# Kernel tuning notes

Measured on AMD Instinct MI355X. Metric: run time of the kernel, lower is better.

## Reference

```python
import jax, jax.numpy as jnp
import numpy as np

B, N, IN_F, OUT_F, H = 16, 1024, 256, 256, 4
D = OUT_F // H  # head_dim = 64
NEG_SLOPE = 0.2


def setup_inputs() -> dict:
    key = jax.random.key(0)
    k1, k2, k3 = jax.random.split(key, 3)
    h = jax.random.normal(k1, (B, N, IN_F), dtype=jnp.float32)
    mask = jnp.ones((B, N), dtype=jnp.int32)
    W = jax.random.normal(k2, (OUT_F, IN_F), dtype=jnp.float32) * (1.0 / np.sqrt(IN_F))
    a = jax.random.normal(k3, (2 * D, 1), dtype=jnp.float32) * 0.1
    return {"h": h, "mask": mask, "W": W, "a": a}


def reference(h, mask, W, a):
    # Wh = h @ W.T -> (B, N, OUT_F) -> (B, H, N, D)
    Wh = jnp.einsum('bnf,of->bno', h, W)
    Wh = Wh.reshape(h.shape[0], h.shape[1], H, D).transpose(0, 2, 1, 3)
    # Additive split: cat([Wh_i, Wh_j]) @ a == Wh_i @ a1 + Wh_j @ a2 (same math,
    # avoids the O(N^2 * 2D) concat tensor)
    a1 = a[:D, 0]  # (D,)
    a2 = a[D:, 0]  # (D,)
    s1 = jnp.einsum('bhnd,d->bhn', Wh, a1)  # score for node i
    s2 = jnp.einsum('bhnd,d->bhn', Wh, a2)  # score for node j
    e = s1[:, :, :, None] + s2[:, :, None, :]          # (B, H, N, N)
    e = jnp.where(e >= 0, e, NEG_SLOPE * e)            # LeakyReLU(0.2)
    node_mask = mask.astype(bool)                      # (B, N)
    mm = node_mask[:, None, :, None] & node_mask[:, None, None, :]  # (B,1,N,N)
    e = jnp.where(mm, e, -jnp.inf)
    attn = jax.nn.softmax(e, axis=-1)
    # dropout is identity in eval mode
    attn = jnp.where(mm, attn, 0.0)
    h_prime = jnp.einsum('bhij,bhjd->bhid', attn, Wh)  # (B, H, N, D)
    h_prime = h_prime.transpose(0, 2, 1, 3).reshape(h.shape[0], h.shape[1], OUT_F)
    return h_prime * mask.astype(h_prime.dtype)[:, :, None]
```

## Files before the change

### kernel.cpp

```cpp
#include <hip/hip_runtime.h>

typedef short short8 __attribute__((ext_vector_type(8)));
typedef float floatx4 __attribute__((ext_vector_type(4)));
typedef float floatx16 __attribute__((ext_vector_type(16)));
typedef unsigned int u32;

#define NEG_SLOPE 0.2f

__device__ __forceinline__ u32 pk_rtne(float a, float b) {
    u32 ua = __float_as_uint(a); ua += 0x7fffu + ((ua >> 16) & 1u);
    u32 ub = __float_as_uint(b); ub += 0x7fffu + ((ub >> 16) & 1u);
    return __builtin_amdgcn_perm(ub, ua, 0x07060302);
}
__device__ __forceinline__ u32 pk_trunc(float a, float b) {
    return __builtin_amdgcn_perm(__float_as_uint(b), __float_as_uint(a), 0x07060302);
}
__device__ __forceinline__ void gl_lds16(const void* g, void* l) {
    __builtin_amdgcn_global_load_lds((__attribute__((address_space(1))) u32*)(void*)g,
                                     (__attribute__((address_space(3))) u32*)l, 16, 0, 0);
}

__global__ __launch_bounds__(256, 4) void k_wh(
    const float* __restrict__ hin, const int* __restrict__ mask,
    const float* __restrict__ W, const float* __restrict__ a,
    unsigned short* __restrict__ WhF, float2* __restrict__ E1F1,
    float2* __restrict__ E2F2)
{
    __shared__ unsigned short sBF[8 * 4 * 64 * 8];
    __shared__ float sV1[256], sV2[256];

    const int t = threadIdx.x;
    const int bi = blockIdx.x;
    const int mtile = bi & 255, hh = bi >> 8;
    const int m0g = mtile * 64;
    const int b = m0g >> 10, i0 = m0g & 1023;
    const int b4h = b * 4 + hh;
    const int wid = t >> 6, lane = t & 63;
    const int l15 = lane & 15, q = lane >> 4;

    sV1[t] = 0.f;
    sV2[t] = 0.f;
    __syncthreads();

    float vp1[8] = {0, 0, 0, 0, 0, 0, 0, 0};
    float vp2[8] = {0, 0, 0, 0, 0, 0, 0, 0};
    {
        const int c = t & 31;
        const int rb = t >> 5;
#pragma unroll
        for (int i = 0; i < 8; ++i) {
            int row = i * 8 + rb;
            const float* gp = &W[((size_t)(hh * 64 + row)) * 256 + c * 8];
            float4 w0 = *(const float4*)gp;
            float4 w1 = *(const float4*)(gp + 4);
            float a1r = a[row], a2r = a[64 + row];
            vp1[0] += a1r * w0.x; vp1[1] += a1r * w0.y; vp1[2] += a1r * w0.z; vp1[3] += a1r * w0.w;
            vp1[4] += a1r * w1.x; vp1[5] += a1r * w1.y; vp1[6] += a1r * w1.z; vp1[7] += a1r * w1.w;
            vp2[0] += a2r * w0.x; vp2[1] += a2r * w0.y; vp2[2] += a2r * w0.z; vp2[3] += a2r * w0.w;
            vp2[4] += a2r * w1.x; vp2[5] += a2r * w1.y; vp2[6] += a2r * w1.z; vp2[7] += a2r * w1.w;
            uint4 pv;
            pv.x = pk_rtne(w0.x, w0.y); pv.y = pk_rtne(w0.z, w0.w);
            pv.z = pk_rtne(w1.x, w1.y); pv.w = pk_rtne(w1.z, w1.w);
            int kt = c >> 2, qq = c & 3, nt = row >> 4, r15 = row & 15;
            int idx16 = (kt * 4 + nt) * 64 + qq * 16 + r15;
            *(uint4*)&sBF[(idx16 ^ kt) * 8] = pv;
        }
    }
#pragma unroll
    for (int j = 0; j < 8; ++j) {
        vp1[j] += __shfl_xor(vp1[j], 32, 64);
        vp2[j] += __shfl_xor(vp2[j], 32, 64);
    }
    if (lane < 32) {
        const int c = t & 31;
#pragma unroll
        for (int j = 0; j < 8; ++j) {
            atomicAdd(&sV1[c * 8 + j], vp1[j]);
            atomicAdd(&sV2[c * 8 + j], vp2[j]);
        }
    }
    __syncthreads();

    floatx4 acc[4];
#pragma unroll
    for (int nt = 0; nt < 4; ++nt) {
        floatx4 z = {0.f, 0.f, 0.f, 0.f};
        acc[nt] = z;
    }
    float s1a = 0.f, s2a = 0.f;
    const float* hrow = &hin[((size_t)(m0g + wid * 16 + l15)) * 256 + q * 8];
#pragma unroll
    for (int kt = 0; kt < 8; ++kt) {
        float4 h0 = *(const float4*)(hrow + kt * 32);
        float4 h1 = *(const float4*)(hrow + kt * 32 + 4);
        float4 v1a = *(const float4*)&sV1[kt * 32 + q * 8];
        float4 v1b = *(const float4*)&sV1[kt * 32 + q * 8 + 4];
        float4 v2a = *(const float4*)&sV2[kt * 32 + q * 8];
        float4 v2b = *(const float4*)&sV2[kt * 32 + q * 8 + 4];
        s1a += h0.x * v1a.x + h0.y * v1a.y + h0.z * v1a.z + h0.w * v1a.w
             + h1.x * v1b.x + h1.y * v1b.y + h1.z * v1b.z + h1.w * v1b.w;
        s2a += h0.x * v2a.x + h0.y * v2a.y + h0.z * v2a.z + h0.w * v2a.w
             + h1.x * v2b.x + h1.y * v2b.y + h1.z * v2b.z + h1.w * v2b.w;
        union { short8 s; uint4 u; } af;
        af.u.x = pk_rtne(h0.x, h0.y); af.u.y = pk_rtne(h0.z, h0.w);
        af.u.z = pk_rtne(h1.x, h1.y); af.u.w = pk_rtne(h1.z, h1.w);
#pragma unroll
        for (int nt = 0; nt < 4; ++nt) {
            int idx16 = (kt * 4 + nt) * 64 + lane;
            short8 bf = *(const short8*)&sBF[(idx16 ^ kt) * 8];
            acc[nt] = __builtin_amdgcn_mfma_f32_16x16x32_bf16(af.s, bf, acc[nt], 0, 0, 0);
        }
    }

    const int jt16 = (i0 >> 4) + wid;
    const int g = q & 1, jb = (q >> 1) * 4;
#pragma unroll
    for (int nt = 0; nt < 4; ++nt) {
        int nt32 = nt >> 1;
        int l31 = (nt & 1) * 16 + l15;
        uint2 pv;
        pv.x = pk_rtne(acc[nt][0], acc[nt][1]);
        pv.y = pk_rtne(acc[nt][2], acc[nt][3]);
        size_t idx = ((((size_t)b4h * 64 + jt16) * 2 + nt32) * 64 + (g * 32 + l31)) * 8 + jb;
        *(uint2*)&WhF[idx] = pv;
    }

    s1a += __shfl_xor(s1a, 16, 64); s1a += __shfl_xor(s1a, 32, 64);
    s2a += __shfl_xor(s2a, 16, 64); s2a += __shfl_xor(s2a, 32, 64);
    if (lane < 16) {
        int i = i0 + wid * 16 + lane;
        E1F1[(size_t)b4h * 1024 + i] = make_float2(__expf(s1a), __expf(NEG_SLOPE * s1a));
        int mj = mask[b * 1024 + i];
        E2F2[(size_t)b4h * 1024 + i] =
            make_float2(mj ? __expf(s2a) : 0.f, mj ? __expf(NEG_SLOPE * s2a) : 0.f);
    }
}

__global__ __launch_bounds__(256, 4) void k_attn(
    const int* __restrict__ mask,
    const unsigned short* __restrict__ WhF,
    const float2* __restrict__ E1F1, const float2* __restrict__ E2F2,
    float* __restrict__ out)
{
    __shared__ float2 sEF[1024];
    __shared__ float sRed[2][64][49];

    const int t = threadIdx.x;
    const int bi = blockIdx.x;
    const int b4h = bi & 63, ib = bi >> 6;
    const int b = b4h >> 2, hh = b4h & 3;
    const int i0 = ib * 64;
    const int wid = t >> 6, lane = t & 63;
    const int l31 = lane & 31, g = lane >> 5;
    const int rg = wid & 1, jh = wid >> 1;
    const int iw = i0 + rg * 32;

    {
        const char* src = (const char*)(E2F2 + (size_t)b4h * 1024);
        gl_lds16(src + t * 16, (char*)sEF + t * 16);
        gl_lds16(src + 4096 + t * 16, (char*)sEF + 4096 + t * 16);
    }

    float2 e1 = E1F1[(size_t)b4h * 1024 + iw + l31];
    const float E1 = e1.x, F1 = e1.y;

    floatx16 acc0, acc1, accL;
#pragma unroll
    for (int r = 0; r < 16; ++r) { acc0[r] = 0.f; acc1[r] = 0.f; accL[r] = 0.f; }
    const short ob = (short)0x3F80;
    const short8 ones = {ob, ob, ob, ob, ob, ob, ob, ob};

    const char* gbase = (const char*)WhF + (size_t)b4h * 131072 + (size_t)lane * 16;
    const int cb = jh * 32;

    short8 ga0 = *(const short8*)(gbase + (size_t)cb * 2048);
    short8 ga1 = *(const short8*)(gbase + (size_t)cb * 2048 + 1024);
    short8 gb0 = *(const short8*)(gbase + (size_t)(cb + 1) * 2048);
    short8 gb1 = *(const short8*)(gbase + (size_t)(cb + 1) * 2048 + 1024);

    __syncthreads();

    float4 nA0, nA1, nB0, nB1;
    {
        const float4* pA = (const float4*)&sEF[cb * 16 + g * 4];
        const float4* pB = (const float4*)&sEF[cb * 16 + 8 + g * 4];
        nA0 = pA[0]; nA1 = pA[1]; nB0 = pB[0]; nB1 = pB[1];
    }

#pragma unroll 4
    for (int cr = 0; cr < 32; cr += 2) {
        {
            const float4 eA0 = nA0, eA1 = nA1, eB0 = nB0, eB1 = nB1;
            const int cn = cb + ((cr + 1) & 31);
            const float4* pA = (const float4*)&sEF[cn * 16 + g * 4];
            const float4* pB = (const float4*)&sEF[cn * 16 + 8 + g * 4];
            nA0 = pA[0]; nA1 = pA[1]; nB0 = pB[0]; nB1 = pB[1];
            const short8 bf0 = ga0, bf1 = ga1;
            const int cg = cb + ((cr + 2) & 31);
            ga0 = *(const short8*)(gbase + (size_t)cg * 2048);
            ga1 = *(const short8*)(gbase + (size_t)cg * 2048 + 1024);
            float w0 = fmaxf(E1 * eA0.x, F1 * eA0.y);
            float w1 = fmaxf(E1 * eA0.z, F1 * eA0.w);
            float w2 = fmaxf(E1 * eA1.x, F1 * eA1.y);
            float w3 = fmaxf(E1 * eA1.z, F1 * eA1.w);
            float w4 = fmaxf(E1 * eB0.x, F1 * eB0.y);
            float w5 = fmaxf(E1 * eB0.z, F1 * eB0.w);
            float w6 = fmaxf(E1 * eB1.x, F1 * eB1.y);
            float w7 = fmaxf(E1 * eB1.z, F1 * eB1.w);
            union { short8 s; u32 u[4]; } af;
            af.u[0] = pk_trunc(w0, w1);
            af.u[1] = pk_trunc(w2, w3);
            af.u[2] = pk_trunc(w4, w5);
            af.u[3] = pk_trunc(w6, w7);
            acc0 = __builtin_amdgcn_mfma_f32_32x32x16_bf16(af.s, bf0, acc0, 0, 0, 0);
            acc1 = __builtin_amdgcn_mfma_f32_32x32x16_bf16(af.s, bf1, acc1, 0, 0, 0);
            accL = __builtin_amdgcn_mfma_f32_32x32x16_bf16(af.s, ones, accL, 0, 0, 0);
        }
        {
            const float4 eA0 = nA0, eA1 = nA1, eB0 = nB0, eB1 = nB1;
            const int cn = cb + ((cr + 2) & 31);
            const float4* pA = (const float4*)&sEF[cn * 16 + g * 4];
            const float4* pB = (const float4*)&sEF[cn * 16 + 8 + g * 4];
            nA0 = pA[0]; nA1 = pA[1]; nB0 = pB[0]; nB1 = pB[1];
            const short8 bf0 = gb0, bf1 = gb1;
            const int cg = cb + ((cr + 3) & 31);
            gb0 = *(const short8*)(gbase + (size_t)cg * 2048);
            gb1 = *(const short8*)(gbase + (size_t)cg * 2048 + 1024);
            float w0 = fmaxf(E1 * eA0.x, F1 * eA0.y);
            float w1 = fmaxf(E1 * eA0.z, F1 * eA0.w);
            float w2 = fmaxf(E1 * eA1.x, F1 * eA1.y);
            float w3 = fmaxf(E1 * eA1.z, F1 * eA1.w);
            float w4 = fmaxf(E1 * eB0.x, F1 * eB0.y);
            float w5 = fmaxf(E1 * eB0.z, F1 * eB0.w);
            float w6 = fmaxf(E1 * eB1.x, F1 * eB1.y);
            float w7 = fmaxf(E1 * eB1.z, F1 * eB1.w);
            union { short8 s; u32 u[4]; } af;
            af.u[0] = pk_trunc(w0, w1);
            af.u[1] = pk_trunc(w2, w3);
            af.u[2] = pk_trunc(w4, w5);
            af.u[3] = pk_trunc(w6, w7);
            acc0 = __builtin_amdgcn_mfma_f32_32x32x16_bf16(af.s, bf0, acc0, 0, 0, 0);
            acc1 = __builtin_amdgcn_mfma_f32_32x32x16_bf16(af.s, bf1, acc1, 0, 0, 0);
            accL = __builtin_amdgcn_mfma_f32_32x32x16_bf16(af.s, ones, accL, 0, 0, 0);
        }
    }

    if (jh == 1) {
        float* d = &sRed[rg][lane][0];
#pragma unroll
        for (int r = 0; r < 16; ++r) {
            d[r] = acc0[r]; d[16 + r] = acc1[r]; d[32 + r] = accL[r];
        }
    }
    __syncthreads();
    if (jh == 0) {
        const float* d = &sRed[rg][lane][0];
#pragma unroll
        for (int r = 0; r < 16; ++r) {
            acc0[r] += d[r]; acc1[r] += d[16 + r]; accL[r] += d[32 + r];
        }
#pragma unroll
        for (int r = 0; r < 16; ++r) {
            int row = (r & 3) + 8 * (r >> 2) + 4 * g;
            int i = iw + row;
            float l = accL[r];
            int mi = mask[b * 1024 + i];
            float inv = (mi && l > 0.f) ? 1.0f / l : 0.f;
            size_t o = ((size_t)(b * 1024 + i)) * 256 + hh * 64;
            out[o + l31] = acc0[r] * inv;
            out[o + 32 + l31] = acc1[r] * inv;
        }
    }
}

extern "C" void kernel_launch(void* const* d_in, const int* in_sizes, int n_in,
                              void* d_out, int out_size, void* d_ws, size_t ws_size,
                              hipStream_t stream) {
    const float* h = (const float*)d_in[0];
    const int* mask = (const int*)d_in[1];
    const float* W = (const float*)d_in[2];
    const float* a = (const float*)d_in[3];
    float* out = (float*)d_out;

    unsigned short* WhF = (unsigned short*)d_ws;
    float2* E1F1 = (float2*)((char*)d_ws + (size_t)64 * 64 * 2 * 64 * 8 * 2);
    float2* E2F2 = E1F1 + 64 * 1024;

    hipLaunchKernelGGL(k_wh, dim3(1024), dim3(256), 0, stream, h, mask, W, a, WhF, E1F1, E2F2);
    hipLaunchKernelGGL(k_attn, dim3(1024), dim3(256), 0, stream, mask, WhF, E1F1, E2F2, out);
}
```

Baseline: 103.2 us.

## Precompute bf16 W fragments and attention projection vectors in a separate prep kernel

Moves the per-head conversion of W to bf16 MFMA fragment layout and the W^T·a projection vectors into a small 4-block prep kernel that writes them to workspace. k_wh then reads B fragments and projection vectors straight from global memory instead of rebuilding them in LDS in every one of its 1024 blocks. This removes the redundant per-block W loads, reductions, atomics and barriers, but adds a kernel launch with little parallelism and makes the MFMA B operands come from global or cache rather than LDS.

```diff
diff --git a/kernel.cpp b/kernel.cpp
--- a/kernel.cpp
+++ b/kernel.cpp
@@ -20,15 +20,66 @@
                                      (__attribute__((address_space(3))) u32*)l, 16, 0, 0);
 }
 
+__global__ __launch_bounds__(256, 4) void k_prep(
+    const float* __restrict__ W, const float* __restrict__ a,
+    unsigned short* __restrict__ WFg, float* __restrict__ V1g,
+    float* __restrict__ V2g)
+{
+    __shared__ float sV1[256], sV2[256];
+    const int t = threadIdx.x;
+    const int hh = blockIdx.x;
+    const int lane = t & 63;
+
+    sV1[t] = 0.f;
+    sV2[t] = 0.f;
+    __syncthreads();
+
+    float vp1[8] = {0, 0, 0, 0, 0, 0, 0, 0};
+    float vp2[8] = {0, 0, 0, 0, 0, 0, 0, 0};
+    const int c = t & 31;
+    const int rb = t >> 5;
+#pragma unroll
+    for (int i = 0; i < 8; ++i) {
+        int row = i * 8 + rb;
+        const float* gp = &W[((size_t)(hh * 64 + row)) * 256 + c * 8];
+        float4 w0 = *(const float4*)gp;
+        float4 w1 = *(const float4*)(gp + 4);
+        float a1r = a[row], a2r = a[64 + row];
+        vp1[0] += a1r * w0.x; vp1[1] += a1r * w0.y; vp1[2] += a1r * w0.z; vp1[3] += a1r * w0.w;
+        vp1[4] += a1r * w1.x; vp1[5] += a1r * w1.y; vp1[6] += a1r * w1.z; vp1[7] += a1r * w1.w;
+        vp2[0] += a2r * w0.x; vp2[1] += a2r * w0.y; vp2[2] += a2r * w0.z; vp2[3] += a2r * w0.w;
+        vp2[4] += a2r * w1.x; vp2[5] += a2r * w1.y; vp2[6] += a2r * w1.z; vp2[7] += a2r * w1.w;
+        uint4 pv;
+        pv.x = pk_rtne(w0.x, w0.y); pv.y = pk_rtne(w0.z, w0.w);
+        pv.z = pk_rtne(w1.x, w1.y); pv.w = pk_rtne(w1.z, w1.w);
+        int kt = c >> 2, qq = c & 3, nt = row >> 4, r15 = row & 15;
+        int idx16 = (kt * 4 + nt) * 64 + qq * 16 + r15;
+        *(uint4*)&WFg[((size_t)hh * 2048 + idx16) * 8] = pv;
+    }
+#pragma unroll
+    for (int j = 0; j < 8; ++j) {
+        vp1[j] += __shfl_xor(vp1[j], 32, 64);
+        vp2[j] += __shfl_xor(vp2[j], 32, 64);
+    }
+    if (lane < 32) {
+#pragma unroll
+        for (int j = 0; j < 8; ++j) {
+            atomicAdd(&sV1[c * 8 + j], vp1[j]);
+            atomicAdd(&sV2[c * 8 + j], vp2[j]);
+        }
+    }
+    __syncthreads();
+    V1g[hh * 256 + t] = sV1[t];
+    V2g[hh * 256 + t] = sV2[t];
+}
+
 __global__ __launch_bounds__(256, 4) void k_wh(
     const float* __restrict__ hin, const int* __restrict__ mask,
-    const float* __restrict__ W, const float* __restrict__ a,
+    const unsigned short* __restrict__ WFg, const float* __restrict__ V1g,
+    const float* __restrict__ V2g,
     unsigned short* __restrict__ WhF, float2* __restrict__ E1F1,
     float2* __restrict__ E2F2)
 {
-    __shared__ unsigned short sBF[8 * 4 * 64 * 8];
-    __shared__ float sV1[256], sV2[256];
-
     const int t = threadIdx.x;
     const int bi = blockIdx.x;
     const int mtile = bi & 255, hh = bi >> 8;
@@ -38,49 +89,6 @@
     const int wid = t >> 6, lane = t & 63;
     const int l15 = lane & 15, q = lane >> 4;
 
-    sV1[t] = 0.f;
-    sV2[t] = 0.f;
-    __syncthreads();
-
-    float vp1[8] = {0, 0, 0, 0, 0, 0, 0, 0};
-    float vp2[8] = {0, 0, 0, 0, 0, 0, 0, 0};
-    {
-        const int c = t & 31;
-        const int rb = t >> 5;
-#pragma unroll
-        for (int i = 0; i < 8; ++i) {
-            int row = i * 8 + rb;
-            const float* gp = &W[((size_t)(hh * 64 + row)) * 256 + c * 8];
-            float4 w0 = *(const float4*)gp;
-            float4 w1 = *(const float4*)(gp + 4);
-            float a1r = a[row], a2r = a[64 + row];
-            vp1[0] += a1r * w0.x; vp1[1] += a1r * w0.y; vp1[2] += a1r * w0.z; vp1[3] += a1r * w0.w;
-            vp1[4] += a1r * w1.x; vp1[5] += a1r * w1.y; vp1[6] += a1r * w1.z; vp1[7] += a1r * w1.w;
-            vp2[0] += a2r * w0.x; vp2[1] += a2r * w0.y; vp2[2] += a2r * w0.z; vp2[3] += a2r * w0.w;
-            vp2[4] += a2r * w1.x; vp2[5] += a2r * w1.y; vp2[6] += a2r * w1.z; vp2[7] += a2r * w1.w;
-            uint4 pv;
-            pv.x = pk_rtne(w0.x, w0.y); pv.y = pk_rtne(w0.z, w0.w);
-            pv.z = pk_rtne(w1.x, w1.y); pv.w = pk_rtne(w1.z, w1.w);
-            int kt = c >> 2, qq = c & 3, nt = row >> 4, r15 = row & 15;
-            int idx16 = (kt * 4 + nt) * 64 + qq * 16 + r15;
-            *(uint4*)&sBF[(idx16 ^ kt) * 8] = pv;
-        }
-    }
-#pragma unroll
-    for (int j = 0; j < 8; ++j) {
-        vp1[j] += __shfl_xor(vp1[j], 32, 64);
-        vp2[j] += __shfl_xor(vp2[j], 32, 64);
-    }
-    if (lane < 32) {
-        const int c = t & 31;
-#pragma unroll
-        for (int j = 0; j < 8; ++j) {
-            atomicAdd(&sV1[c * 8 + j], vp1[j]);
-            atomicAdd(&sV2[c * 8 + j], vp2[j]);
-        }
-    }
-    __syncthreads();
-
     floatx4 acc[4];
 #pragma unroll
     for (int nt = 0; nt < 4; ++nt) {
@@ -89,14 +97,17 @@
     }
     float s1a = 0.f, s2a = 0.f;
     const float* hrow = &hin[((size_t)(m0g + wid * 16 + l15)) * 256 + q * 8];
+    const unsigned short* wf = &WFg[(size_t)hh * 16384 + (size_t)lane * 8];
+    const float* v1 = &V1g[hh * 256 + q * 8];
+    const float* v2 = &V2g[hh * 256 + q * 8];
 #pragma unroll
     for (int kt = 0; kt < 8; ++kt) {
         float4 h0 = *(const float4*)(hrow + kt * 32);
         float4 h1 = *(const float4*)(hrow + kt * 32 + 4);
-        float4 v1a = *(const float4*)&sV1[kt * 32 + q * 8];
-        float4 v1b = *(const float4*)&sV1[kt * 32 + q * 8 + 4];
-        float4 v2a = *(const float4*)&sV2[kt * 32 + q * 8];
-        float4 v2b = *(const float4*)&sV2[kt * 32 + q * 8 + 4];
+        float4 v1a = *(const float4*)(v1 + kt * 32);
+        float4 v1b = *(const float4*)(v1 + kt * 32 + 4);
+        float4 v2a = *(const float4*)(v2 + kt * 32);
+        float4 v2b = *(const float4*)(v2 + kt * 32 + 4);
         s1a += h0.x * v1a.x + h0.y * v1a.y + h0.z * v1a.z + h0.w * v1a.w
              + h1.x * v1b.x + h1.y * v1b.y + h1.z * v1b.z + h1.w * v1b.w;
         s2a += h0.x * v2a.x + h0.y * v2a.y + h0.z * v2a.z + h0.w * v2a.w
@@ -106,8 +117,7 @@
         af.u.z = pk_rtne(h1.x, h1.y); af.u.w = pk_rtne(h1.z, h1.w);
 #pragma unroll
         for (int nt = 0; nt < 4; ++nt) {
-            int idx16 = (kt * 4 + nt) * 64 + lane;
-            short8 bf = *(const short8*)&sBF[(idx16 ^ kt) * 8];
+            short8 bf = *(const short8*)(wf + (size_t)(kt * 4 + nt) * 512);
             acc[nt] = __builtin_amdgcn_mfma_f32_16x16x32_bf16(af.s, bf, acc[nt], 0, 0, 0);
         }
     }
@@ -283,9 +293,13 @@
     float* out = (float*)d_out;
 
     unsigned short* WhF = (unsigned short*)d_ws;
-    float2* E1F1 = (float2*)((char*)d_ws + (size_t)64 * 64 * 2 * 64 * 8 * 2);
+    float2* E1F1 = (float2*)((char*)d_ws + (size_t)8 * 1024 * 1024);
     float2* E2F2 = E1F1 + 64 * 1024;
-
-    hipLaunchKernelGGL(k_wh, dim3(1024), dim3(256), 0, stream, h, mask, W, a, WhF, E1F1, E2F2);
+    unsigned short* WFg = (unsigned short*)((char*)d_ws + (size_t)9 * 1024 * 1024);
+    float* V1g = (float*)((char*)WFg + 4 * 16384 * sizeof(unsigned short));
+    float* V2g = V1g + 1024;
+
+    hipLaunchKernelGGL(k_prep, dim3(4), dim3(256), 0, stream, W, a, WFg, V1g, V2g);
+    hipLaunchKernelGGL(k_wh, dim3(1024), dim3(256), 0, stream, h, mask, WFg, V1g, V2g, WhF, E1F1, E2F2);
     hipLaunchKernelGGL(k_attn, dim3(1024), dim3(256), 0, stream, mask, WhF, E1F1, E2F2, out);
 }
```

Result: slower. 107.9 us (+4.6%).
